# Kernel optimization log

Measured on AMD Instinct MI355X. Metric: run time of the kernel, lower is better.

The kernel has to match this reference:

```python
import jax, jax.numpy as jnp
import numpy as np

D_MODEL = 1024
N_HEADS = 16
HEAD_DIM = D_MODEL // N_HEADS


def setup_inputs() -> dict:
    key = jax.random.key(0)
    ks = jax.random.split(key, 5)
    s = 0.02  # small init scale to keep softmax numerics reasonable
    x = jax.random.normal(ks[0], (4, 2048, D_MODEL), dtype=jnp.float32)
    w_qkv = jax.random.normal(ks[1], (D_MODEL, 3 * D_MODEL), dtype=jnp.float32) * s
    b_qkv = jnp.zeros((3 * D_MODEL,), dtype=jnp.float32)
    w_proj = jax.random.normal(ks[2], (D_MODEL, D_MODEL), dtype=jnp.float32) * s
    b_proj = jnp.zeros((D_MODEL,), dtype=jnp.float32)
    return {"x": x, "w_qkv": w_qkv, "b_qkv": b_qkv, "w_proj": w_proj, "b_proj": b_proj}


def reference(x, w_qkv, b_qkv, w_proj, b_proj):
    B, T, C = x.shape
    scale = 1.0 / np.sqrt(HEAD_DIM)
    qkv = x @ w_qkv + b_qkv                               # [B,T,3C]
    qkv = qkv.reshape(B, T, 3, N_HEADS, HEAD_DIM)
    q = qkv[:, :, 0].transpose(0, 2, 1, 3)               # [B,H,T,D]
    k = qkv[:, :, 1].transpose(0, 2, 1, 3)
    v = qkv[:, :, 2].transpose(0, 2, 1, 3)
    att = jnp.einsum('bhqd,bhkd->bhqk', q, k) * scale    # [B,H,T,T]
    causal = jnp.tril(jnp.ones((T, T), dtype=bool))
    att = jnp.where(causal, att, -jnp.inf)
    att = jax.nn.softmax(att, axis=-1)
    y = jnp.einsum('bhqk,bhkd->bhqd', att, v)            # [B,H,T,D]
    y = y.transpose(0, 2, 1, 3).reshape(B, T, C)
    y = y @ w_proj + b_proj
    return y
```

## Files before the change

### kernel.cpp

```cpp
#include <hip/hip_runtime.h>
#include <stdint.h>

#define BATCH 4
#define SEQ 2048
#define DMODEL 1024
#define NHEADS 16
#define HDIM 64
#define MROWS (BATCH * SEQ)

typedef float floatx4 __attribute__((ext_vector_type(4)));
typedef __bf16 bf16x8 __attribute__((ext_vector_type(8)));
typedef __bf16 bf16x4 __attribute__((ext_vector_type(4)));
typedef short short8 __attribute__((ext_vector_type(8)));

__device__ __forceinline__ unsigned short f32_to_bf16(float f) {
    union { float f; unsigned int u; } c; c.f = f;
    unsigned int u = c.u;
    unsigned int r = (u + 0x7FFFu + ((u >> 16) & 1u)) >> 16;
    return (unsigned short)r;
}

__device__ __forceinline__ void async_ld16(const void* g, void* l) {
    __builtin_amdgcn_global_load_lds(
        (const __attribute__((address_space(1))) unsigned int*)g,
        (__attribute__((address_space(3))) unsigned int*)l, 16, 0, 0);
}

__global__ __launch_bounds__(256) void prep_kernel(
    const float* __restrict__ x, unsigned short* __restrict__ xb,
    const float* __restrict__ w_qkv, unsigned short* __restrict__ wqkvT,
    const float* __restrict__ w_proj, unsigned short* __restrict__ wprojT) {
    const int gx = blockIdx.x, gy = blockIdx.y;
    const int tx = threadIdx.x, ty = threadIdx.y;
    if (gx < 256) {
        int i = (gx * 32 + gy) * 256 + ty * 32 + tx;
        float4 v = ((const float4*)x)[i];
        ushort4 o;
        o.x = f32_to_bf16(v.x); o.y = f32_to_bf16(v.y);
        o.z = f32_to_bf16(v.z); o.w = f32_to_bf16(v.w);
        ((ushort4*)xb)[i] = o;
        return;
    }
    __shared__ float tile[32][33];
    const float* in; unsigned short* out; int N, bx;
    if (gx < 352) { in = w_qkv; out = wqkvT; N = 3072; bx = (gx - 256) * 32; }
    else          { in = w_proj; out = wprojT; N = 1024; bx = (gx - 352) * 32; }
    const int by = gy * 32;
#pragma unroll
    for (int i = 0; i < 4; ++i)
        tile[ty + i * 8][tx] = in[(size_t)(by + ty + i * 8) * N + bx + tx];
    __syncthreads();
#pragma unroll
    for (int i = 0; i < 4; ++i)
        out[(size_t)(bx + ty + i * 8) * DMODEL + by + tx] = f32_to_bf16(tile[tx][ty + i * 8]);
}

template <int EPI>
__global__ __launch_bounds__(256, 3) void gemm_bt(
    const unsigned short* __restrict__ A, const unsigned short* __restrict__ Bt,
    const float* __restrict__ bias, float* __restrict__ Cout,
    unsigned short* __restrict__ Qo, unsigned short* __restrict__ Ko,
    unsigned short* __restrict__ Vo, int M, int N, int K) {
    __shared__ __align__(16) unsigned short SM[24576];
    const int tid = threadIdx.x;
    const int lane = tid & 63;
    const int w = tid >> 6;
    const int wm = w & 1, wn = w >> 1;
    const int quad = lane >> 4, l16 = lane & 15;

    const int nbx = gridDim.x;
    const int nwg = nbx * gridDim.y;
    const int lin = blockIdx.y * nbx + blockIdx.x;
    const int swz = (lin & 7) * (nwg >> 3) + (lin >> 3);
    const int m0 = (swz / nbx) * 128;
    const int n0 = (swz % nbx) * 128;
    const int fsw = (l16 >> 1) & 3;

    const int idx0 = tid, idx1 = tid + 256;
    const int row0 = idx0 >> 2, row1 = idx1 >> 2;
    const int cg0 = (idx0 & 3) ^ ((row0 >> 1) & 3);
    const int cg1 = (idx1 & 3) ^ ((row1 >> 1) & 3);
    const unsigned short* Ar0 = &A[(size_t)(m0 + row0) * K + cg0 * 8];
    const unsigned short* Ar1 = &A[(size_t)(m0 + row1) * K + cg1 * 8];
    const unsigned short* Br0 = &Bt[(size_t)(n0 + row0) * K + cg0 * 8];
    const unsigned short* Br1 = &Bt[(size_t)(n0 + row1) * K + cg1 * 8];

    floatx4 acc[4][4];
#pragma unroll
    for (int mt = 0; mt < 4; ++mt)
#pragma unroll
        for (int nt = 0; nt < 4; ++nt) acc[mt][nt] = (floatx4){0.f, 0.f, 0.f, 0.f};

    async_ld16(Ar0, &SM[idx0 * 8]);
    async_ld16(Br0, &SM[12288 + idx0 * 8]);
    async_ld16(Ar1, &SM[idx1 * 8]);
    async_ld16(Br1, &SM[12288 + idx1 * 8]);
    async_ld16(Ar0 + 32, &SM[4096 + idx0 * 8]);
    async_ld16(Br0 + 32, &SM[16384 + idx0 * 8]);
    async_ld16(Ar1 + 32, &SM[4096 + idx1 * 8]);
    async_ld16(Br1 + 32, &SM[16384 + idx1 * 8]);

    const int nk = K >> 5;
    int bcur = 0, bpre = 2;
    for (int kt = 0; kt < nk; ++kt) {
        if (kt + 2 < nk)
            asm volatile("s_waitcnt vmcnt(4)" ::: "memory");
        else
            asm volatile("s_waitcnt vmcnt(0)" ::: "memory");
        __builtin_amdgcn_s_barrier();
        asm volatile("" ::: "memory");

        if (kt + 2 < nk) {
            const int ko = (kt + 2) << 5;
            async_ld16(Ar0 + ko, &SM[bpre * 4096 + idx0 * 8]);
            async_ld16(Br0 + ko, &SM[12288 + bpre * 4096 + idx0 * 8]);
            async_ld16(Ar1 + ko, &SM[bpre * 4096 + idx1 * 8]);
            async_ld16(Br1 + ko, &SM[12288 + bpre * 4096 + idx1 * 8]);
        }

        bf16x8 aF[4], bF[4];
#pragma unroll
        for (int mt = 0; mt < 4; ++mt)
            aF[mt] = *(const bf16x8*)&SM[bcur * 4096 +
                                         (wm * 64 + mt * 16 + l16) * 32 + (quad ^ fsw) * 8];
#pragma unroll
        for (int nt = 0; nt < 4; ++nt)
            bF[nt] = *(const bf16x8*)&SM[12288 + bcur * 4096 +
                                         (wn * 64 + nt * 16 + l16) * 32 + (quad ^ fsw) * 8];
#pragma unroll
        for (int mt = 0; mt < 4; ++mt)
#pragma unroll
            for (int nt = 0; nt < 4; ++nt)
                acc[mt][nt] = __builtin_amdgcn_mfma_f32_16x16x32_bf16(
                    aF[mt], bF[nt], acc[mt][nt], 0, 0, 0);

        bcur = (bcur == 2) ? 0 : bcur + 1;
        bpre = (bpre == 2) ? 0 : bpre + 1;
    }

    if (EPI == 0 && n0 >= 2048) {
        const int hbase = (n0 - 2048) >> 6;
        const int bb = m0 >> 11, t0 = m0 & 2047;
        __syncthreads();
#pragma unroll
        for (int mt = 0; mt < 4; ++mt)
#pragma unroll
            for (int nt = 0; nt < 4; ++nt)
#pragma unroll
                for (int r = 0; r < 4; ++r) {
                    int tl = wm * 64 + mt * 16 + quad * 4 + r;
                    int nl = wn * 64 + nt * 16 + l16;
                    int c2 = (tl & 64) | ((tl & 15) << 2) | ((tl >> 4) & 3);
                    float v = acc[mt][nt][r] + bias[n0 + nl];
                    SM[nl * 132 + c2] = f32_to_bf16(v);
                }
        __syncthreads();
        const int rr = tid >> 1, hh = tid & 1;
        const int head = hbase + (rr >> 6), d = rr & 63;
        unsigned short* drow = Vo + ((size_t)(bb * NHEADS + head)) * SEQ * HDIM +
                               (size_t)d * SEQ + t0 + hh * 64;
        const unsigned short* srow = &SM[rr * 132 + hh * 64];
#pragma unroll
        for (int c = 0; c < 16; ++c)
            *(bf16x4*)&drow[c * 4] = *(const bf16x4*)&srow[c * 4];
        return;
    }

#pragma unroll
    for (int mt = 0; mt < 4; ++mt)
#pragma unroll
        for (int nt = 0; nt < 4; ++nt)
#pragma unroll
            for (int r = 0; r < 4; ++r) {
                int m = m0 + wm * 64 + mt * 16 + quad * 4 + r;
                int n = n0 + wn * 64 + nt * 16 + l16;
                float v = acc[mt][nt][r] + bias[n];
                if (EPI == 1) {
                    Cout[(size_t)m * N + n] = v;
                } else {
                    int sel = n >> 10, c = n & 1023;
                    int head = c >> 6, d = c & 63;
                    int bb = m >> 11, t = m & 2047;
                    unsigned short* dst = sel == 0 ? Qo : Ko;
                    dst[((((size_t)bb * NHEADS + head) * SEQ + t) << 6) + d] = f32_to_bf16(v);
                }
            }
}

__device__ __forceinline__ void strip_body(
    int kb, int rowb, int quad, int l16,
    const bf16x8 (&qf)[2][2], const unsigned short* Kb, const unsigned short* Vb,
    unsigned short* Pw, bf16x8 ones, float csc,
    floatx4 (&o)[2][4], floatx4 (&lsum)[2]) {
    floatx4 s[2][4];
#pragma unroll
    for (int mt = 0; mt < 2; ++mt)
#pragma unroll
        for (int nt = 0; nt < 4; ++nt) s[mt][nt] = (floatx4){0.f, 0.f, 0.f, 0.f};
#pragma unroll
    for (int kk = 0; kk < 2; ++kk) {
        bf16x8 kf[4];
#pragma unroll
        for (int nt = 0; nt < 4; ++nt)
            kf[nt] = *(const bf16x8*)&Kb[(nt * 16 + l16) * 64 +
                                         ((kk * 4 + quad) ^ (l16 & 7)) * 8];
        __builtin_amdgcn_s_setprio(1);
#pragma unroll
        for (int nt = 0; nt < 4; ++nt)
#pragma unroll
            for (int mt = 0; mt < 2; ++mt)
                s[mt][nt] = __builtin_amdgcn_mfma_f32_16x16x32_bf16(
                    qf[mt][kk], kf[nt], s[mt][nt], 0, 0, 0);
        __builtin_amdgcn_s_setprio(0);
    }

    if ((kb * 64 + 63) > rowb) {
#pragma unroll
        for (int mt = 0; mt < 2; ++mt)
#pragma unroll
            for (int nt = 0; nt < 4; ++nt)
#pragma unroll
                for (int r = 0; r < 4; ++r) {
                    int key = kb * 64 + nt * 16 + l16;
                    int qrow = rowb + mt * 16 + quad * 4 + r;
                    if (key > qrow) s[mt][nt][r] = -INFINITY;
                }
    }

#pragma unroll
    for (int mt = 0; mt < 2; ++mt)
#pragma unroll
        for (int nt = 0; nt < 4; ++nt)
#pragma unroll
            for (int r = 0; r < 4; ++r)
                s[mt][nt][r] = __builtin_amdgcn_exp2f(s[mt][nt][r] * csc);

#pragma unroll
    for (int mt = 0; mt < 2; ++mt)
#pragma unroll
        for (int r = 0; r < 4; ++r) {
            int prow = mt * 16 + quad * 4 + r;
            int unit = l16 ^ (prow & 14);
            floatx4 t = {s[mt][0][r], s[mt][1][r], s[mt][2][r], s[mt][3][r]};
            bf16x4 pv = __builtin_convertvector(t, bf16x4);
            *(bf16x4*)&Pw[prow * 64 + unit * 4] = pv;
        }

#pragma unroll
    for (int kk = 0; kk < 2; ++kk) {
        bf16x8 af[2];
#pragma unroll
        for (int mt = 0; mt < 2; ++mt) {
            int prow = mt * 16 + l16;
            int u2 = (kk * 8 + quad * 2) ^ (l16 & 14);
            af[mt] = *(const bf16x8*)&Pw[prow * 64 + u2 * 4];
        }
        bf16x8 vf[4];
#pragma unroll
        for (int nt = 0; nt < 4; ++nt)
            vf[nt] = *(const bf16x8*)&Vb[(nt * 16 + l16) * 64 +
                                         ((kk * 4 + quad) ^ (l16 & 7)) * 8];
        __builtin_amdgcn_s_setprio(1);
#pragma unroll
        for (int nt = 0; nt < 4; ++nt)
#pragma unroll
            for (int mt = 0; mt < 2; ++mt)
                o[mt][nt] = __builtin_amdgcn_mfma_f32_16x16x32_bf16(
                    af[mt], vf[nt], o[mt][nt], 0, 0, 0);
#pragma unroll
        for (int mt = 0; mt < 2; ++mt)
            lsum[mt] = __builtin_amdgcn_mfma_f32_16x16x32_bf16(
                af[mt], ones, lsum[mt], 0, 0, 0);
        __builtin_amdgcn_s_setprio(0);
    }
}

__global__ __launch_bounds__(256, 2) void attn_kernel(
    const unsigned short* __restrict__ Qg, const unsigned short* __restrict__ Kg,
    const unsigned short* __restrict__ Vtg, unsigned short* __restrict__ Yatt) {
    __shared__ __align__(16) unsigned short Kb2[3][4096];
    __shared__ __align__(16) unsigned short Vb2[3][4096];
    __shared__ __align__(16) unsigned short Ps[4][2048];

    const int tid = threadIdx.x;
    const int lane = tid & 63;
    const int w = tid >> 6;
    const int quad = lane >> 4, l16 = lane & 15;
    const int bh = blockIdx.x;
    const int by = blockIdx.y;
    const int sA = by * 4 + w;
    const size_t base = (size_t)bh * SEQ * HDIM;
    const int bIdx = bh >> 4, h = bh & 15;
    unsigned short* Pw = &Ps[w][0];
    const float csc = 0.18033688f;

    const int lrow = lane >> 3;
    const int lch = (lane & 7) ^ lrow;

    short8 osv = {0x3F80, 0x3F80, 0x3F80, 0x3F80, 0x3F80, 0x3F80, 0x3F80, 0x3F80};
    bf16x8 ones = __builtin_bit_cast(bf16x8, osv);

    const int rowbA = sA * 32;
    const int rowbB = (63 - sA) * 32;
    const int tA = 2 * by + 2, tB = 32 - 2 * by;
    const int kmaxB = tA > tB ? tA : tB;
    const int lastA = sA >> 1;
    const int lastB = (2047 - 32 * sA) >> 6;

    const unsigned short* Ktg = Kg + base;
    const unsigned short* Vtg_t = Vtg + base;
    const int i0 = w * 2, i1 = w * 2 + 1;
    const int kof0 = (i0 * 8 + lrow) * 64 + lch * 8;
    const int kof1 = (i1 * 8 + lrow) * 64 + lch * 8;
    const size_t vof0 = (size_t)(i0 * 8 + lrow) * SEQ + lch * 8;
    const size_t vof1 = (size_t)(i1 * 8 + lrow) * SEQ + lch * 8;
    const int ld0 = i0 * 512 + lane * 8;
    const int ld1 = i1 * 512 + lane * 8;

    bf16x8 qfA[2][2], qfB[2][2];
#pragma unroll
    for (int mt = 0; mt < 2; ++mt)
#pragma unroll
        for (int kk = 0; kk < 2; ++kk) {
            qfA[mt][kk] = *(const bf16x8*)&Qg[base + (size_t)(rowbA + mt * 16 + l16) * 64 +
                                              kk * 32 + quad * 8];
            qfB[mt][kk] = *(const bf16x8*)&Qg[base + (size_t)(rowbB + mt * 16 + l16) * 64 +
                                              kk * 32 + quad * 8];
        }
    asm volatile("" ::: "memory");

    floatx4 lsumA[2], lsumB[2];
    floatx4 oA[2][4], oB[2][4];
#pragma unroll
    for (int mt = 0; mt < 2; ++mt) {
        lsumA[mt] = (floatx4){0.f, 0.f, 0.f, 0.f};
        lsumB[mt] = (floatx4){0.f, 0.f, 0.f, 0.f};
#pragma unroll
        for (int nt = 0; nt < 4; ++nt) {
            oA[mt][nt] = (floatx4){0.f, 0.f, 0.f, 0.f};
            oB[mt][nt] = (floatx4){0.f, 0.f, 0.f, 0.f};
        }
    }

    async_ld16(Ktg + kof0, &Kb2[0][ld0]);
    async_ld16(Vtg_t + vof0, &Vb2[0][ld0]);
    async_ld16(Ktg + kof1, &Kb2[0][ld1]);
    async_ld16(Vtg_t + vof1, &Vb2[0][ld1]);
    async_ld16(Ktg + 64 * HDIM + kof0, &Kb2[1][ld0]);
    async_ld16(Vtg_t + 64 + vof0, &Vb2[1][ld0]);
    async_ld16(Ktg + 64 * HDIM + kof1, &Kb2[1][ld1]);
    async_ld16(Vtg_t + 64 + vof1, &Vb2[1][ld1]);

    int bcur = 0, bpre = 2;
    for (int kb = 0; kb < kmaxB; ++kb) {
        if (kb + 2 < kmaxB)
            asm volatile("s_waitcnt vmcnt(4)" ::: "memory");
        else
            asm volatile("s_waitcnt vmcnt(0)" ::: "memory");
        __builtin_amdgcn_s_barrier();
        asm volatile("" ::: "memory");

        if (kb + 2 < kmaxB) {
            const unsigned short* Kt2 = Ktg + (size_t)(kb + 2) * 64 * HDIM;
            const unsigned short* Vt2 = Vtg_t + (kb + 2) * 64;
            async_ld16(Kt2 + kof0, &Kb2[bpre][ld0]);
            async_ld16(Vt2 + vof0, &Vb2[bpre][ld0]);
            async_ld16(Kt2 + kof1, &Kb2[bpre][ld1]);
            async_ld16(Vt2 + vof1, &Vb2[bpre][ld1]);
        }

        if (kb <= lastA)
            strip_body(kb, rowbA, quad, l16, qfA, &Kb2[bcur][0], &Vb2[bcur][0],
                       Pw, ones, csc, oA, lsumA);
        if (kb <= lastB)
            strip_body(kb, rowbB, quad, l16, qfB, &Kb2[bcur][0], &Vb2[bcur][0],
                       Pw, ones, csc, oB, lsumB);

        bcur = (bcur == 2) ? 0 : bcur + 1;
        bpre = (bpre == 2) ? 0 : bpre + 1;
    }

#pragma unroll
    for (int mt = 0; mt < 2; ++mt)
#pragma unroll
        for (int r = 0; r < 4; ++r) {
            float invA = 1.0f / lsumA[mt][r];
            float invB = 1.0f / lsumB[mt][r];
            int qrowA = rowbA + mt * 16 + quad * 4 + r;
            int qrowB = rowbB + mt * 16 + quad * 4 + r;
#pragma unroll
            for (int nt = 0; nt < 4; ++nt) {
                Yatt[((size_t)(bIdx * SEQ + qrowA) << 10) + h * 64 + nt * 16 + l16] =
                    f32_to_bf16(oA[mt][nt][r] * invA);
                Yatt[((size_t)(bIdx * SEQ + qrowB) << 10) + h * 64 + nt * 16 + l16] =
                    f32_to_bf16(oB[mt][nt][r] * invB);
            }
        }
}

extern "C" void kernel_launch(void* const* d_in, const int* in_sizes, int n_in,
                              void* d_out, int out_size, void* d_ws, size_t ws_size,
                              hipStream_t stream) {
    const float* x = (const float*)d_in[0];
    const float* w_qkv = (const float*)d_in[1];
    const float* b_qkv = (const float*)d_in[2];
    const float* w_proj = (const float*)d_in[3];
    const float* b_proj = (const float*)d_in[4];
    float* out = (float*)d_out;

    char* ws = (char*)d_ws;
    unsigned short* xb     = (unsigned short*)(ws);
    unsigned short* wqkvT  = (unsigned short*)(ws + 16777216);
    unsigned short* wprojT = (unsigned short*)(ws + 23068672);
    unsigned short* Qb     = (unsigned short*)(ws + 25165824);
    unsigned short* Kb     = (unsigned short*)(ws + 41943040);
    unsigned short* Yatt   = (unsigned short*)(ws + 75497472);
    unsigned short* Vt     = (unsigned short*)(ws + 92274688);

    prep_kernel<<<dim3(384, 32), dim3(32, 8), 0, stream>>>(x, xb, w_qkv, wqkvT,
                                                           w_proj, wprojT);
    gemm_bt<0><<<dim3(24, 64), 256, 0, stream>>>(xb, wqkvT, b_qkv, nullptr, Qb, Kb, Vt,
                                                 MROWS, 3 * DMODEL, DMODEL);
    attn_kernel<<<dim3(64, 8), 256, 0, stream>>>(Qb, Kb, Vt, Yatt);
    gemm_bt<1><<<dim3(8, 64), 256, 0, stream>>>(Yatt, wprojT, b_proj, out, nullptr, nullptr,
                                                nullptr, MROWS, DMODEL, DMODEL);
}
```

Before: 236.1 us.

## Share K/V LDS fragment loads across both query strips in attention loop

Restructures the per-block attention body so that K and V fragments are read from LDS once per key block and reused by both query strips (A and B), instead of each strip reloading them. QK^T/softmax packing for both strips now runs before the PV accumulation, which requires separate P scratch buffers per strip and doubles that LDS allocation. This trades redundant LDS reads for higher register pressure (kf[2][4] held live) and more shared memory, which may affect occupancy at 2 blocks per CU.

```diff
diff --git a/kernel.cpp b/kernel.cpp
--- a/kernel.cpp
+++ b/kernel.cpp
@@ -187,11 +187,10 @@
             }
 }
 
-__device__ __forceinline__ void strip_body(
+__device__ __forceinline__ void qkt_pack(
     int kb, int rowb, int quad, int l16,
-    const bf16x8 (&qf)[2][2], const unsigned short* Kb, const unsigned short* Vb,
-    unsigned short* Pw, bf16x8 ones, float csc,
-    floatx4 (&o)[2][4], floatx4 (&lsum)[2]) {
+    const bf16x8 (&qf)[2][2], const bf16x8 (&kf)[2][4],
+    unsigned short* Pw, float csc) {
     floatx4 s[2][4];
 #pragma unroll
     for (int mt = 0; mt < 2; ++mt)
@@ -199,18 +198,13 @@
         for (int nt = 0; nt < 4; ++nt) s[mt][nt] = (floatx4){0.f, 0.f, 0.f, 0.f};
 #pragma unroll
     for (int kk = 0; kk < 2; ++kk) {
-        bf16x8 kf[4];
-#pragma unroll
-        for (int nt = 0; nt < 4; ++nt)
-            kf[nt] = *(const bf16x8*)&Kb[(nt * 16 + l16) * 64 +
-                                         ((kk * 4 + quad) ^ (l16 & 7)) * 8];
         __builtin_amdgcn_s_setprio(1);
 #pragma unroll
         for (int nt = 0; nt < 4; ++nt)
 #pragma unroll
             for (int mt = 0; mt < 2; ++mt)
                 s[mt][nt] = __builtin_amdgcn_mfma_f32_16x16x32_bf16(
-                    qf[mt][kk], kf[nt], s[mt][nt], 0, 0, 0);
+                    qf[mt][kk], kf[kk][nt], s[mt][nt], 0, 0, 0);
         __builtin_amdgcn_s_setprio(0);
     }
 
@@ -245,34 +239,30 @@
             bf16x4 pv = __builtin_convertvector(t, bf16x4);
             *(bf16x4*)&Pw[prow * 64 + unit * 4] = pv;
         }
-
-#pragma unroll
-    for (int kk = 0; kk < 2; ++kk) {
-        bf16x8 af[2];
-#pragma unroll
-        for (int mt = 0; mt < 2; ++mt) {
-            int prow = mt * 16 + l16;
-            int u2 = (kk * 8 + quad * 2) ^ (l16 & 14);
-            af[mt] = *(const bf16x8*)&Pw[prow * 64 + u2 * 4];
-        }
-        bf16x8 vf[4];
-#pragma unroll
-        for (int nt = 0; nt < 4; ++nt)
-            vf[nt] = *(const bf16x8*)&Vb[(nt * 16 + l16) * 64 +
-                                         ((kk * 4 + quad) ^ (l16 & 7)) * 8];
-        __builtin_amdgcn_s_setprio(1);
-#pragma unroll
-        for (int nt = 0; nt < 4; ++nt)
-#pragma unroll
-            for (int mt = 0; mt < 2; ++mt)
-                o[mt][nt] = __builtin_amdgcn_mfma_f32_16x16x32_bf16(
-                    af[mt], vf[nt], o[mt][nt], 0, 0, 0);
+}
+
+__device__ __forceinline__ void pv_acc(
+    int kk, int quad, int l16, const unsigned short* Pw, const bf16x8 (&vf)[4],
+    bf16x8 ones, floatx4 (&o)[2][4], floatx4 (&lsum)[2]) {
+    bf16x8 af[2];
+#pragma unroll
+    for (int mt = 0; mt < 2; ++mt) {
+        int prow = mt * 16 + l16;
+        int u2 = (kk * 8 + quad * 2) ^ (l16 & 14);
+        af[mt] = *(const bf16x8*)&Pw[prow * 64 + u2 * 4];
+    }
+    __builtin_amdgcn_s_setprio(1);
+#pragma unroll
+    for (int nt = 0; nt < 4; ++nt)
 #pragma unroll
         for (int mt = 0; mt < 2; ++mt)
-            lsum[mt] = __builtin_amdgcn_mfma_f32_16x16x32_bf16(
-                af[mt], ones, lsum[mt], 0, 0, 0);
-        __builtin_amdgcn_s_setprio(0);
-    }
+            o[mt][nt] = __builtin_amdgcn_mfma_f32_16x16x32_bf16(
+                af[mt], vf[nt], o[mt][nt], 0, 0, 0);
+#pragma unroll
+    for (int mt = 0; mt < 2; ++mt)
+        lsum[mt] = __builtin_amdgcn_mfma_f32_16x16x32_bf16(
+            af[mt], ones, lsum[mt], 0, 0, 0);
+    __builtin_amdgcn_s_setprio(0);
 }
 
 __global__ __launch_bounds__(256, 2) void attn_kernel(
@@ -280,7 +270,8 @@
     const unsigned short* __restrict__ Vtg, unsigned short* __restrict__ Yatt) {
     __shared__ __align__(16) unsigned short Kb2[3][4096];
     __shared__ __align__(16) unsigned short Vb2[3][4096];
-    __shared__ __align__(16) unsigned short Ps[4][2048];
+    __shared__ __align__(16) unsigned short PsA[4][2048];
+    __shared__ __align__(16) unsigned short PsB[4][2048];
 
     const int tid = threadIdx.x;
     const int lane = tid & 63;
@@ -291,7 +282,8 @@
     const int sA = by * 4 + w;
     const size_t base = (size_t)bh * SEQ * HDIM;
     const int bIdx = bh >> 4, h = bh & 15;
-    unsigned short* Pw = &Ps[w][0];
+    unsigned short* PwA = &PsA[w][0];
+    unsigned short* PwB = &PsB[w][0];
     const float csc = 0.18033688f;
 
     const int lrow = lane >> 3;
@@ -369,12 +361,34 @@
             async_ld16(Vt2 + vof1, &Vb2[bpre][ld1]);
         }
 
-        if (kb <= lastA)
-            strip_body(kb, rowbA, quad, l16, qfA, &Kb2[bcur][0], &Vb2[bcur][0],
-                       Pw, ones, csc, oA, lsumA);
-        if (kb <= lastB)
-            strip_body(kb, rowbB, quad, l16, qfB, &Kb2[bcur][0], &Vb2[bcur][0],
-                       Pw, ones, csc, oB, lsumB);
+        const unsigned short* Kb = &Kb2[bcur][0];
+        const unsigned short* Vb = &Vb2[bcur][0];
+        const bool doA = kb <= lastA;
+        const bool doB = kb <= lastB;
+
+        if (doA || doB) {
+            bf16x8 kf[2][4];
+#pragma unroll
+            for (int kk = 0; kk < 2; ++kk)
+#pragma unroll
+                for (int nt = 0; nt < 4; ++nt)
+                    kf[kk][nt] = *(const bf16x8*)&Kb[(nt * 16 + l16) * 64 +
+                                                     ((kk * 4 + quad) ^ (l16 & 7)) * 8];
+
+            if (doA) qkt_pack(kb, rowbA, quad, l16, qfA, kf, PwA, csc);
+            if (doB) qkt_pack(kb, rowbB, quad, l16, qfB, kf, PwB, csc);
+
+#pragma unroll
+            for (int kk = 0; kk < 2; ++kk) {
+                bf16x8 vf[4];
+#pragma unroll
+                for (int nt = 0; nt < 4; ++nt)
+                    vf[nt] = *(const bf16x8*)&Vb[(nt * 16 + l16) * 64 +
+                                                 ((kk * 4 + quad) ^ (l16 & 7)) * 8];
+                if (doA) pv_acc(kk, quad, l16, PwA, vf, ones, oA, lsumA);
+                if (doB) pv_acc(kk, quad, l16, PwB, vf, ones, oB, lsumB);
+            }
+        }
 
         bcur = (bcur == 2) ? 0 : bcur + 1;
         bpre = (bpre == 2) ? 0 : bpre + 1;
```

Result: no change. 239.4 us (+1.4%).
